# Optimization experiments

Hardware: AMD Instinct MI355X
Metric: run time of the kernel (lower is better)

## Reference

```python
import jax, jax.numpy as jnp
import numpy as np

N = 50000      # nodes per graph
E = 800000     # directed edges per graph
D_IN, C1, C2, C3, K = 96, 64, 32, 16, 16  # K = tensor_neurons (Linear(16,16) forces 16)


def setup_inputs() -> dict:
    key = jax.random.key(0)
    ks = jax.random.split(key, 18)
    def w(k, shape, scale=0.1):
        return (jax.random.normal(k, shape, jnp.float32) * scale)
    return {
        "features_1": jax.random.normal(ks[0], (N, D_IN), jnp.float32),
        "features_2": jax.random.normal(ks[1], (N, D_IN), jnp.float32),
        "edges_1": jax.random.randint(ks[2], (2, E), 0, N),
        "edges_2": jax.random.randint(ks[3], (2, E), 0, N),
        # GCN layer params (PyG GCNConv: X @ W then normalized aggregation, then + b)
        "W1": w(ks[4], (D_IN, C1)), "b1": jnp.zeros((C1,), jnp.float32),
        "W2": w(ks[5], (C1, C2)),  "b2": jnp.zeros((C2,), jnp.float32),
        "W3": w(ks[6], (C2, C3)),  "b3": jnp.zeros((C3,), jnp.float32),
        # Attention pooling weight matrix [C3, C3]
        "Wa": w(ks[7], (C3, C3)),
        # Tensor network: bilinear tensor [C3, C3, K], block [K, 2*C3], bias [K]
        "Wt": w(ks[8], (C3, C3, K)),
        "Wb": w(ks[9], (K, 2 * C3)),
        "bt": w(ks[10], (K,)),
        # fully_connected_first Linear(16,16) and scoring Linear(16,1)
        "Wfc": w(ks[11], (K, 16)), "bfc": jnp.zeros((16,), jnp.float32),
        "Wsc": w(ks[12], (16, 1)), "bsc": jnp.zeros((1,), jnp.float32),
    }


def gcn_conv(x, src, dst, W, b):
    # PyG GCNConv with self-loops: D^-1/2 (A+I) D^-1/2 (X W) + b
    h = x @ W                                   # [N, C]
    ones = jnp.ones(src.shape[0], h.dtype)
    deg = jax.ops.segment_sum(ones, dst, num_segments=N) + 1.0   # in-degree + self loop
    dinv = jax.lax.rsqrt(deg)                   # [N]
    coef = dinv[src] * dinv[dst]                # [E]
    agg = jax.ops.segment_sum(h[src] * coef[:, None], dst, num_segments=N)
    return agg + h * (dinv * dinv)[:, None] + b  # self-loop term has norm dinv_i^2


def encode(x, edges, W1, b1, W2, b2, W3, b3):
    src, dst = edges[0], edges[1]
    x = jax.nn.relu(gcn_conv(x, src, dst, W1, b1))  # dropout is a no-op in eval mode
    x = jax.nn.relu(gcn_conv(x, src, dst, W2, b2))
    return gcn_conv(x, src, dst, W3, b3)


def attention_pool(x, Wa):
    # SimGNN AttentionModule: c = tanh(mean(x Wa)); s = sigmoid(x c); rep = x^T s
    c = jnp.tanh(jnp.mean(x @ Wa, axis=0))      # [C3]
    s = jax.nn.sigmoid(x @ c)                   # [N]
    return x.T @ s                              # [C3]


def reference(features_1, features_2, edges_1, edges_2,
              W1, b1, W2, b2, W3, b3, Wa, Wt, Wb, bt, Wfc, bfc, Wsc, bsc):
    h1 = encode(features_1, edges_1, W1, b1, W2, b2, W3, b3)
    h2 = encode(features_2, edges_2, W1, b1, W2, b2, W3, b3)
    e1 = attention_pool(h1, Wa)                 # [C3]
    e2 = attention_pool(h2, Wa)                 # [C3]
    # Tensor network scoring
    bilinear = jnp.einsum('i,ijk,j->k', e1, Wt, e2)        # [K]
    block = Wb @ jnp.concatenate([e1, e2])                 # [K]
    scores = jax.nn.relu(bilinear + block + bt)            # [K]
    scores = jnp.tanh(scores @ Wfc + bfc)                  # [16]
    score = jax.nn.sigmoid(scores @ Wsc + bsc)             # [1]
    return score
```

## Files before the change

kernel.cpp:

```cpp
#include <hip/hip_runtime.h>
#include <hip/hip_bf16.h>

#define TPB 256
#define SH 6
#define BW 64

typedef unsigned short u16;
typedef __attribute__((ext_vector_type(8))) __bf16 bf16x8;
typedef __attribute__((ext_vector_type(4))) float f32x4;

__device__ __forceinline__ u16 f_to_bf(float f) {
    unsigned u = __float_as_uint(f);
    return (u16)((u + 0x7fff + ((u >> 16) & 1)) >> 16);
}
__device__ __forceinline__ void facc(float4& a, float4 v) {
    a.x += v.x; a.y += v.y; a.z += v.z; a.w += v.w;
}

__device__ __forceinline__ bool swz_block(int nblk, int& g, int& bx) {
    int blk = blockIdx.x;
    int j = blk & 7;
    g = j >> 2;
    bx = (blk >> 3) * 4 + (j & 3);
    return bx < nblk;
}

__device__ __forceinline__ void acc8_add(float* __restrict__ a, uint4 d) {
    a[0] += __uint_as_float(d.x << 16);
    a[1] += __uint_as_float(d.x & 0xffff0000u);
    a[2] += __uint_as_float(d.y << 16);
    a[3] += __uint_as_float(d.y & 0xffff0000u);
    a[4] += __uint_as_float(d.z << 16);
    a[5] += __uint_as_float(d.z & 0xffff0000u);
    a[6] += __uint_as_float(d.w << 16);
    a[7] += __uint_as_float(d.w & 0xffff0000u);
}

template <int C>
__device__ __forceinline__ void gather_sum16(const u16* __restrict__ HW,
                                             const int* __restrict__ col,
                                             int e, int c8, int ps, int pe,
                                             float* __restrict__ acc) {
    int p = ps;
    for (; p + 8 <= pe; p += 8) {
        int j[4];
        uint4 d[4];
#pragma unroll
        for (int r = 0; r < 4; r++) j[r] = col[p + 2 * r + e];
#pragma unroll
        for (int r = 0; r < 4; r++) d[r] = *(const uint4*)&HW[(size_t)j[r] * C + c8 * 8];
#pragma unroll
        for (int r = 0; r < 4; r++) acc8_add(acc, d[r]);
    }
    for (; p + 2 <= pe; p += 2) {
        int j = col[p + e];
        acc8_add(acc, *(const uint4*)&HW[(size_t)j * C + c8 * 8]);
    }
    if (p < pe && e == 0) {
        int j = col[p];
        acc8_add(acc, *(const uint4*)&HW[(size_t)j * C + c8 * 8]);
    }
}

__device__ __forceinline__ void red8(float* __restrict__ a, int mask, int width) {
#pragma unroll
    for (int i = 0; i < 8; i++) a[i] += __shfl_xor(a[i], mask, width);
}


__global__ void bucket_scatter_kernel(const int* __restrict__ e0, const int* __restrict__ e1,
                                      int E, int* __restrict__ bcur,
                                      int* __restrict__ ebuf0, int* __restrict__ ebuf1,
                                      int nbuk, int cap) {
    int g = blockIdx.y;
    const int* src = g ? e1 : e0;
    const int* dst = src + E;
    int* ebuf = g ? ebuf1 : ebuf0;
    int* bu = bcur + g * 1024;
    __shared__ int hist[1024];
    for (int t = threadIdx.x; t < 1024; t += TPB) hist[t] = 0;
    __syncthreads();
    int base = blockIdx.x * 4096;
    int pk[16], bk[16], rk[16];
#pragma unroll
    for (int k = 0; k < 16; k++) {
        int e = base + k * TPB + (int)threadIdx.x;
        bk[k] = -1;
        if (e < E) {
            int s = src[e], d = dst[e];
            int b = d >> SH;
            bk[k] = b;
            pk[k] = (s << SH) | (d & (BW - 1));
            rk[k] = atomicAdd(&hist[b], 1);
        }
    }
    __syncthreads();
    for (int t = threadIdx.x; t < nbuk; t += TPB) {
        int h = hist[t];
        hist[t] = h ? atomicAdd(&bu[t], h) : 0;
    }
    __syncthreads();
#pragma unroll
    for (int k = 0; k < 16; k++)
        if (bk[k] >= 0) {
            int pos = hist[bk[k]] + rk[k];
            if (pos < cap) ebuf[(size_t)bk[k] * cap + pos] = pk[k];
        }
}

__global__ void bucket_csr_kernel(const int* __restrict__ ebuf0, const int* __restrict__ ebuf1,
                                  const int* __restrict__ bcur, int n, int cap,
                                  int* __restrict__ soff0, int* __restrict__ soff1,
                                  int* __restrict__ eoff0, int* __restrict__ eoff1,
                                  float* __restrict__ dinv0, float* __restrict__ dinv1,
                                  int* __restrict__ col0, int* __restrict__ col1) {
    int g = blockIdx.y;
    int b = blockIdx.x;
    const int* ebuf = g ? ebuf1 : ebuf0;
    int* soff = g ? soff1 : soff0;
    int* eoff = g ? eoff1 : eoff0;
    float* dinv = g ? dinv1 : dinv0;
    int* col = g ? col1 : col0;
    __shared__ int h[BW], nb[BW], nrank[BW];
    int tid = threadIdx.x;
    if (tid < BW) h[tid] = 0;
    __syncthreads();
    int s = b * cap;
    int cnt = min(bcur[g * 1024 + b], cap);
    int e = s + cnt;
    for (int i = s + tid; i < e; i += TPB)
        atomicAdd(&h[ebuf[i] & (BW - 1)], 1);
    __syncthreads();
    if (tid < BW) {
        int v = h[tid];
        int x = v;
        for (int d = 1; d < BW; d <<= 1) {
            int u = __shfl_up(x, d, 64);
            if (tid >= d) x += u;
        }
        int base = s + x - v;
        nb[tid] = base;
        nrank[tid] = 0;
        int node = b * BW + tid;
        if (node < n) {
            soff[node] = base;
            eoff[node] = base + v;
            dinv[node] = rsqrtf((float)v + 1.0f);
        }
    }
    __syncthreads();
    for (int i = s + tid; i < e; i += TPB) {
        int p = ebuf[i];
        int lo = p & (BW - 1);
        int r = atomicAdd(&nrank[lo], 1);
        col[nb[lo] + r] = p >> SH;
    }
}


template <int CIN, int COUT>
__global__ void matmul_kernel(const float* __restrict__ X0, const float* __restrict__ X1,
                              const float* __restrict__ W,
                              const float* __restrict__ dinv0, const float* __restrict__ dinv1,
                              u16* __restrict__ Y0, u16* __restrict__ Y1, int n) {
    constexpr int CINP = CIN + 8;
    constexpr int NT = COUT / 16;
    constexpr int KT = CIN / 32;
    __shared__ u16 Xs[64 * CINP];
    __shared__ u16 Wt[COUT * CINP];

    int g = blockIdx.y;
    const float* X = g ? X1 : X0;
    const float* dinv = g ? dinv1 : dinv0;
    u16* Y = g ? Y1 : Y0;
    int nb0 = blockIdx.x * 64;

    for (int i = threadIdx.x; i < 64 * (CIN / 4); i += TPB) {
        int nn = i / (CIN / 4), kc = i % (CIN / 4);
        float4 v = make_float4(0.f, 0.f, 0.f, 0.f);
        if (nb0 + nn < n) v = *(const float4*)&X[(size_t)(nb0 + nn) * CIN + 4 * kc];
        ushort4 b;
        b.x = f_to_bf(v.x); b.y = f_to_bf(v.y); b.z = f_to_bf(v.z); b.w = f_to_bf(v.w);
        *(ushort4*)&Xs[nn * CINP + 4 * kc] = b;
    }
    for (int i = threadIdx.x; i < CIN * (COUT / 4); i += TPB) {
        int k = i / (COUT / 4), nc4 = i % (COUT / 4);
        float4 v = *(const float4*)&W[(size_t)k * COUT + 4 * nc4];
        Wt[(4 * nc4 + 0) * CINP + k] = f_to_bf(v.x);
        Wt[(4 * nc4 + 1) * CINP + k] = f_to_bf(v.y);
        Wt[(4 * nc4 + 2) * CINP + k] = f_to_bf(v.z);
        Wt[(4 * nc4 + 3) * CINP + k] = f_to_bf(v.w);
    }
    __syncthreads();

    int lane = threadIdx.x & 63;
    int w = threadIdx.x >> 6;
    int m = lane & 15;
    int quad = lane >> 4;

    f32x4 acc[NT];
#pragma unroll
    for (int t = 0; t < NT; t++) acc[t] = (f32x4){0.f, 0.f, 0.f, 0.f};
#pragma unroll
    for (int kt = 0; kt < KT; kt++) {
        int k0 = kt * 32 + quad * 8;
        bf16x8 a = *(const bf16x8*)&Xs[(w * 16 + m) * CINP + k0];
#pragma unroll
        for (int t = 0; t < NT; t++) {
            bf16x8 b = *(const bf16x8*)&Wt[(t * 16 + m) * CINP + k0];
            acc[t] = __builtin_amdgcn_mfma_f32_16x16x32_bf16(a, b, acc[t], 0, 0, 0);
        }
    }
#pragma unroll
    for (int r = 0; r < 4; r++) {
        int node = nb0 + w * 16 + quad * 4 + r;
        if (node < n) {
            float d = dinv[node];
#pragma unroll
            for (int t = 0; t < NT; t++)
                Y[(size_t)node * COUT + t * 16 + m] = f_to_bf(acc[t][r] * d);
        }
    }
}


template <int C, int SPLIT, int COUT2>
__global__ __launch_bounds__(TPB, 2)
void agg_mm_kernel(const u16* __restrict__ HW0, const u16* __restrict__ HW1,
                   const int* __restrict__ soff0, const int* __restrict__ soff1,
                   const int* __restrict__ eoff0, const int* __restrict__ eoff1,
                   const int* __restrict__ col0, const int* __restrict__ col1,
                   const float* __restrict__ dinv0, const float* __restrict__ dinv1,
                   const float* __restrict__ bias, const float* __restrict__ W2,
                   u16* __restrict__ Y0, u16* __restrict__ Y1, int n, int nblk) {
    constexpr int CHUNKS = C / 8;
    constexpr int GRP = 2 * CHUNKS;
    constexpr int TPN = GRP * SPLIT;
    constexpr int CP = C + 8;
    constexpr int NT2 = COUT2 / 16;
    constexpr int KT2 = C / 32;
    __shared__ __align__(16) u16 HsB[16 * CP];
    __shared__ __align__(16) u16 WtB[COUT2 * CP];

    int g, bx;
    if (!swz_block(nblk, g, bx)) return;
    const u16* HW = g ? HW1 : HW0;
    const int* soff = g ? soff1 : soff0;
    const int* eoff = g ? eoff1 : eoff0;
    const int* col = g ? col1 : col0;
    const float* dinv = g ? dinv1 : dinv0;
    u16* Y = g ? Y1 : Y0;

    for (int idx = threadIdx.x; idx < C * COUT2; idx += TPB) {
        int k = idx / COUT2, nc = idx % COUT2;
        WtB[nc * CP + k] = f_to_bf(W2[idx]);
    }

    int nl = threadIdx.x >> 4;
    int part = threadIdx.x & 15;
    int sp = part / GRP;
    int gl = part % GRP;
    int e = gl / CHUNKS;
    int c8 = gl % CHUNKS;
    int node = bx * 16 + nl;

    float acc[8];
#pragma unroll
    for (int i = 0; i < 8; i++) acc[i] = 0.f;
    float o8[8];
#pragma unroll
    for (int i = 0; i < 8; i++) o8[i] = 0.f;

    if (node < n) {
        int s = soff[node], en = eoff[node];
        int len = en - s;
        int chunk = (len + SPLIT - 1) / SPLIT;
        int ps = s + sp * chunk;
        int pe = min(ps + chunk, en);
        gather_sum16<C>(HW, col, e, c8, ps, pe, acc);
        red8(acc, CHUNKS, TPN);
#pragma unroll
        for (int m = GRP; m < TPN; m <<= 1) red8(acc, m, TPN);
        if (part < CHUNKS) {
            float di = dinv[node];
            uint4 sv = *(const uint4*)&HW[(size_t)node * C + part * 8];
            float4 b0 = *(const float4*)&bias[part * 8];
            float4 b1 = *(const float4*)&bias[part * 8 + 4];
            o8[0] = fmaxf(di * (acc[0] + __uint_as_float(sv.x << 16)) + b0.x, 0.f);
            o8[1] = fmaxf(di * (acc[1] + __uint_as_float(sv.x & 0xffff0000u)) + b0.y, 0.f);
            o8[2] = fmaxf(di * (acc[2] + __uint_as_float(sv.y << 16)) + b0.z, 0.f);
            o8[3] = fmaxf(di * (acc[3] + __uint_as_float(sv.y & 0xffff0000u)) + b0.w, 0.f);
            o8[4] = fmaxf(di * (acc[4] + __uint_as_float(sv.z << 16)) + b1.x, 0.f);
            o8[5] = fmaxf(di * (acc[5] + __uint_as_float(sv.z & 0xffff0000u)) + b1.y, 0.f);
            o8[6] = fmaxf(di * (acc[6] + __uint_as_float(sv.w << 16)) + b1.z, 0.f);
            o8[7] = fmaxf(di * (acc[7] + __uint_as_float(sv.w & 0xffff0000u)) + b1.w, 0.f);
        }
    }
    if (part < CHUNKS) {
        uint4 hv;
        hv.x = (unsigned)f_to_bf(o8[0]) | ((unsigned)f_to_bf(o8[1]) << 16);
        hv.y = (unsigned)f_to_bf(o8[2]) | ((unsigned)f_to_bf(o8[3]) << 16);
        hv.z = (unsigned)f_to_bf(o8[4]) | ((unsigned)f_to_bf(o8[5]) << 16);
        hv.w = (unsigned)f_to_bf(o8[6]) | ((unsigned)f_to_bf(o8[7]) << 16);
        *(uint4*)&HsB[nl * CP + part * 8] = hv;
    }
    __syncthreads();

    int lane = threadIdx.x & 63;
    int w = threadIdx.x >> 6;
    if (w < NT2) {
        int m = lane & 15;
        int quad = lane >> 4;
        f32x4 ac = (f32x4){0.f, 0.f, 0.f, 0.f};
#pragma unroll
        for (int kt = 0; kt < KT2; kt++) {
            int k0 = kt * 32 + quad * 8;
            bf16x8 a = *(const bf16x8*)&HsB[m * CP + k0];
            bf16x8 b = *(const bf16x8*)&WtB[(w * 16 + m) * CP + k0];
            ac = __builtin_amdgcn_mfma_f32_16x16x32_bf16(a, b, ac, 0, 0, 0);
        }
        int base16 = bx * 16;
#pragma unroll
        for (int r = 0; r < 4; r++) {
            int onode = base16 + quad * 4 + r;
            if (onode < n)
                Y[(size_t)onode * COUT2 + w * 16 + m] = f_to_bf(ac[r] * dinv[onode]);
        }
    }
}

__global__ __launch_bounds__(TPB, 2)
void agg16_kernel(const u16* __restrict__ HW0, const u16* __restrict__ HW1,
                  const int* __restrict__ soff0, const int* __restrict__ soff1,
                  const int* __restrict__ eoff0, const int* __restrict__ eoff1,
                  const int* __restrict__ col0, const int* __restrict__ col1,
                  const float* __restrict__ dinv0, const float* __restrict__ dinv1,
                  const float* __restrict__ bias,
                  u16* __restrict__ out0, u16* __restrict__ out1,
                  float* __restrict__ pcol, int n, int nblk) {
    int g, bx;
    if (!swz_block(nblk, g, bx)) return;
    const u16* HW = g ? HW1 : HW0;
    const int* soff = g ? soff1 : soff0;
    const int* eoff = g ? eoff1 : eoff0;
    const int* col = g ? col1 : col0;
    const float* dinv = g ? dinv1 : dinv0;
    u16* outp = g ? out1 : out0;

    int nl = threadIdx.x >> 4;
    int part = threadIdx.x & 15;
    int sp = part >> 2;
    int gl = part & 3;
    int e = gl >> 1;
    int c8 = gl & 1;
    int node = bx * 16 + nl;

    float acc[8];
#pragma unroll
    for (int i = 0; i < 8; i++) acc[i] = 0.f;
    float o8[8];
#pragma unroll
    for (int i = 0; i < 8; i++) o8[i] = 0.f;

    if (node < n) {
        int s = soff[node], en = eoff[node];
        int len = en - s;
        int chunk = (len + 3) >> 2;
        int ps = s + sp * chunk;
        int pe = min(ps + chunk, en);
        gather_sum16<16>(HW, col, e, c8, ps, pe, acc);
        red8(acc, 2, 16);
        red8(acc, 4, 16);
        red8(acc, 8, 16);
        if (part < 2) {
            float di = dinv[node];
            uint4 sv = *(const uint4*)&HW[(size_t)node * 16 + part * 8];
            float4 b0 = *(const float4*)&bias[part * 8];
            float4 b1 = *(const float4*)&bias[part * 8 + 4];
            o8[0] = di * (acc[0] + __uint_as_float(sv.x << 16)) + b0.x;
            o8[1] = di * (acc[1] + __uint_as_float(sv.x & 0xffff0000u)) + b0.y;
            o8[2] = di * (acc[2] + __uint_as_float(sv.y << 16)) + b0.z;
            o8[3] = di * (acc[3] + __uint_as_float(sv.y & 0xffff0000u)) + b0.w;
            o8[4] = di * (acc[4] + __uint_as_float(sv.z << 16)) + b1.x;
            o8[5] = di * (acc[5] + __uint_as_float(sv.z & 0xffff0000u)) + b1.y;
            o8[6] = di * (acc[6] + __uint_as_float(sv.w << 16)) + b1.z;
            o8[7] = di * (acc[7] + __uint_as_float(sv.w & 0xffff0000u)) + b1.w;
            uint4 hv;
            hv.x = (unsigned)f_to_bf(o8[0]) | ((unsigned)f_to_bf(o8[1]) << 16);
            hv.y = (unsigned)f_to_bf(o8[2]) | ((unsigned)f_to_bf(o8[3]) << 16);
            hv.z = (unsigned)f_to_bf(o8[4]) | ((unsigned)f_to_bf(o8[5]) << 16);
            hv.w = (unsigned)f_to_bf(o8[6]) | ((unsigned)f_to_bf(o8[7]) << 16);
            *(uint4*)&outp[(size_t)node * 16 + part * 8] = hv;
        }
    }
    __shared__ float4 sa[TPB], sb[TPB];
    bool hold = (node < n) && (part < 2);
    sa[threadIdx.x] = hold ? make_float4(o8[0], o8[1], o8[2], o8[3])
                           : make_float4(0.f, 0.f, 0.f, 0.f);
    sb[threadIdx.x] = hold ? make_float4(o8[4], o8[5], o8[6], o8[7])
                           : make_float4(0.f, 0.f, 0.f, 0.f);
    __syncthreads();
    if (threadIdx.x < 64) {
        float4 a = sa[threadIdx.x], b = sb[threadIdx.x];
        facc(a, sa[threadIdx.x + 64]);  facc(b, sb[threadIdx.x + 64]);
        facc(a, sa[threadIdx.x + 128]); facc(b, sb[threadIdx.x + 128]);
        facc(a, sa[threadIdx.x + 192]); facc(b, sb[threadIdx.x + 192]);
        sa[threadIdx.x] = a; sb[threadIdx.x] = b;
    }
    __syncthreads();
    if (threadIdx.x < 16) {
        float4 a = sa[threadIdx.x], b = sb[threadIdx.x];
        facc(a, sa[threadIdx.x + 16]); facc(b, sb[threadIdx.x + 16]);
        facc(a, sa[threadIdx.x + 32]); facc(b, sb[threadIdx.x + 32]);
        facc(a, sa[threadIdx.x + 48]); facc(b, sb[threadIdx.x + 48]);
        sa[threadIdx.x] = a; sb[threadIdx.x] = b;
    }
    __syncthreads();
    if (threadIdx.x < 2) {
        float* dst = &pcol[((size_t)g * nblk + bx) * 16 + threadIdx.x * 8];
        *(float4*)&dst[0] = sa[threadIdx.x];
        *(float4*)&dst[4] = sb[threadIdx.x];
    }
}


__global__ void cvec_kernel(const float* __restrict__ pcol, int nb16, float n_inv,
                            const float* __restrict__ Wa, float* __restrict__ cvec) {
    int g = blockIdx.x;
    const float4* p4 = (const float4*)(pcol + (size_t)g * nb16 * 16);
    __shared__ float4 sd[TPB];
    __shared__ float cs[16];
    int c4 = threadIdx.x & 3;
    int row = threadIdx.x >> 2;
    float4 acc = make_float4(0.f, 0.f, 0.f, 0.f);
    for (int r = row; r < nb16; r += 64) facc(acc, p4[(size_t)r * 4 + c4]);
    sd[threadIdx.x] = acc;
    __syncthreads();
    if (threadIdx.x < 64) {
        float4 a = sd[threadIdx.x];
        facc(a, sd[threadIdx.x + 64]);
        facc(a, sd[threadIdx.x + 128]);
        facc(a, sd[threadIdx.x + 192]);
        sd[threadIdx.x] = a;
    }
    __syncthreads();
    if (threadIdx.x < 16) {
        float4 a = sd[threadIdx.x];
        facc(a, sd[threadIdx.x + 16]);
        facc(a, sd[threadIdx.x + 32]);
        facc(a, sd[threadIdx.x + 48]);
        sd[threadIdx.x] = a;
    }
// ... 106 lines not shown
        tvec[t] = tanhf(acc);
    }
    __syncthreads();
    if (t == 0) {
        float acc = bsc[0];
#pragma unroll
        for (int j = 0; j < 16; j++) acc += tvec[j] * Wsc[j];
        out[0] = 1.f / (1.f + __expf(-acc));
    }
}


extern "C" void kernel_launch(void* const* d_in, const int* in_sizes, int n_in,
                              void* d_out, int out_size, void* d_ws, size_t ws_size,
                              hipStream_t stream) {
    const float* X1 = (const float*)d_in[0];
    const float* X2 = (const float*)d_in[1];
    const int* edges1 = (const int*)d_in[2];
    const int* edges2 = (const int*)d_in[3];
    const float* W1 = (const float*)d_in[4];
    const float* b1 = (const float*)d_in[5];
    const float* W2 = (const float*)d_in[6];
    const float* b2 = (const float*)d_in[7];
    const float* W3 = (const float*)d_in[8];
    const float* b3 = (const float*)d_in[9];
    const float* Wa = (const float*)d_in[10];
    const float* Wt = (const float*)d_in[11];
    const float* Wb = (const float*)d_in[12];
    const float* bt = (const float*)d_in[13];
    const float* Wfc = (const float*)d_in[14];
    const float* bfc = (const float*)d_in[15];
    const float* Wsc = (const float*)d_in[16];
    const float* bsc = (const float*)d_in[17];
    float* out = (float*)d_out;

    const int N = in_sizes[0] / 96;
    const int E = in_sizes[2] / 2;
    const int NBUK = (N + BW - 1) / BW;
    int cap = ((2 * (E / NBUK)) + 255) & ~255;
    if (cap < 256) cap = 256;

    char* ws = (char*)d_ws;
    size_t o = 0;
    auto alloc = [&](size_t bytes) {
        void* p = ws + o;
        o += (bytes + 255) & ~(size_t)255;
        return p;
    };
    int* bcur = (int*)alloc((size_t)2 * 1024 * 4);
    int* soff0 = (int*)alloc((size_t)N * 4);
    int* soff1 = (int*)alloc((size_t)N * 4);
    int* eoff0 = (int*)alloc((size_t)N * 4);
    int* eoff1 = (int*)alloc((size_t)N * 4);
    int* col0 = (int*)alloc((size_t)NBUK * cap * 4);
    int* col1 = (int*)alloc((size_t)NBUK * cap * 4);
    int* ebuf0 = (int*)alloc((size_t)NBUK * cap * 4);
    int* ebuf1 = (int*)alloc((size_t)NBUK * cap * 4);
    float* dinv0 = (float*)alloc((size_t)N * 4);
    float* dinv1 = (float*)alloc((size_t)N * 4);
    u16* hwbA0 = (u16*)alloc((size_t)N * 64 * 2);
    u16* hwbA1 = (u16*)alloc((size_t)N * 64 * 2);
    u16* hwbB0 = (u16*)alloc((size_t)N * 32 * 2);
    u16* hwbB1 = (u16*)alloc((size_t)N * 32 * 2);
    u16* hwbC0 = (u16*)alloc((size_t)N * 16 * 2);
    u16* hwbC1 = (u16*)alloc((size_t)N * 16 * 2);
    u16* H30 = (u16*)alloc((size_t)N * 16 * 2);
    u16* H31 = (u16*)alloc((size_t)N * 16 * 2);

    const int gB2 = (E + 4095) / 4096;
    const int g16 = ((size_t)N * 16 + TPB - 1) / TPB;
    const int gSwz = 8 * ((g16 + 3) / 4);
    const int gMM = (N + 63) / 64;
    const int gPool = 256;

    float* pcol = (float*)alloc((size_t)2 * g16 * 16 * 4);
    float* cvecArr = (float*)alloc(32 * 4);
    float* ppool = (float*)alloc((size_t)2 * gPool * 16 * 4);

    hipMemsetAsync(bcur, 0, (size_t)2 * 1024 * 4, stream);

    bucket_scatter_kernel<<<dim3(gB2, 2), TPB, 0, stream>>>(edges1, edges2, E, bcur,
                                                            ebuf0, ebuf1, NBUK, cap);
    bucket_csr_kernel<<<dim3(NBUK, 2), TPB, 0, stream>>>(ebuf0, ebuf1, bcur, N, cap,
                                                         soff0, soff1, eoff0, eoff1,
                                                         dinv0, dinv1, col0, col1);

    matmul_kernel<96, 64><<<dim3(gMM, 2), TPB, 0, stream>>>(X1, X2, W1, dinv0, dinv1,
                                                            hwbA0, hwbA1, N);
    agg_mm_kernel<64, 1, 32><<<gSwz, TPB, 0, stream>>>(
        hwbA0, hwbA1, soff0, soff1, eoff0, eoff1, col0, col1, dinv0, dinv1, b1, W2,
        hwbB0, hwbB1, N, g16);
    agg_mm_kernel<32, 2, 16><<<gSwz, TPB, 0, stream>>>(
        hwbB0, hwbB1, soff0, soff1, eoff0, eoff1, col0, col1, dinv0, dinv1, b2, W3,
        hwbC0, hwbC1, N, g16);
    agg16_kernel<<<gSwz, TPB, 0, stream>>>(
        hwbC0, hwbC1, soff0, soff1, eoff0, eoff1, col0, col1, dinv0, dinv1, b3,
        H30, H31, pcol, N, g16);

    cvec_kernel<<<2, TPB, 0, stream>>>(pcol, g16, 1.0f / (float)N, Wa, cvecArr);
    pool_kernel<<<dim3(gPool, 2), TPB, 0, stream>>>(H30, H31, N, cvecArr, ppool);
    final_kernel<<<1, 256, 0, stream>>>(ppool, gPool, Wt, Wb, bt, Wfc, bfc, Wsc, bsc, out);
}
```

Measured before the change: 256.7 us.

## Store intermediate GCN feature tables in FP8 and regroup gather threads

The per-layer transformed feature tables (X·W scaled by dinv) are now stored as FP8 instead of bf16, halving bytes per gathered neighbor row. Gather threads now load 16 channels per 16-byte load and process 4 edges in parallel per group, with the shuffle reductions adjusted to match. This is meant to cut memory traffic in the bandwidth-bound edge aggregations. The cost is extra conversion instructions and lower precision, which could hurt output accuracy.

Measured after the change: 272.4 us. +6.1%, slower.

```diff
diff --git a/kernel.cpp b/kernel.cpp
--- a/kernel.cpp
+++ b/kernel.cpp
@@ -6,6 +6,7 @@
 #define BW 64
 
 typedef unsigned short u16;
+typedef unsigned char u8;
 typedef __attribute__((ext_vector_type(8))) __bf16 bf16x8;
 typedef __attribute__((ext_vector_type(4))) float f32x4;
 
@@ -13,8 +14,35 @@
     unsigned u = __float_as_uint(f);
     return (u16)((u + 0x7fff + ((u >> 16) & 1)) >> 16);
 }
+__device__ __forceinline__ unsigned pkbf(float a, float b) {
+    return (unsigned)f_to_bf(a) | ((unsigned)f_to_bf(b) << 16);
+}
 __device__ __forceinline__ void facc(float4& a, float4 v) {
     a.x += v.x; a.y += v.y; a.z += v.z; a.w += v.w;
+}
+
+__device__ __forceinline__ u8 f_to_fp8(float f) {
+    return (u8)(__builtin_amdgcn_cvt_pk_fp8_f32(f, f, 0, false) & 0xff);
+}
+__device__ __forceinline__ void dec16(uint4 d, float* __restrict__ f) {
+    auto w = __builtin_amdgcn_cvt_pk_f32_fp8(d.x, false); f[0] = w[0]; f[1] = w[1];
+    w = __builtin_amdgcn_cvt_pk_f32_fp8(d.x, true);  f[2] = w[0];  f[3] = w[1];
+    w = __builtin_amdgcn_cvt_pk_f32_fp8(d.y, false); f[4] = w[0];  f[5] = w[1];
+    w = __builtin_amdgcn_cvt_pk_f32_fp8(d.y, true);  f[6] = w[0];  f[7] = w[1];
+    w = __builtin_amdgcn_cvt_pk_f32_fp8(d.z, false); f[8] = w[0];  f[9] = w[1];
+    w = __builtin_amdgcn_cvt_pk_f32_fp8(d.z, true);  f[10] = w[0]; f[11] = w[1];
+    w = __builtin_amdgcn_cvt_pk_f32_fp8(d.w, false); f[12] = w[0]; f[13] = w[1];
+    w = __builtin_amdgcn_cvt_pk_f32_fp8(d.w, true);  f[14] = w[0]; f[15] = w[1];
+}
+__device__ __forceinline__ void acc16_add(float* __restrict__ a, uint4 d) {
+    float t[16];
+    dec16(d, t);
+#pragma unroll
+    for (int i = 0; i < 16; i++) a[i] += t[i];
+}
+__device__ __forceinline__ void red16(float* __restrict__ a, int mask) {
+#pragma unroll
+    for (int i = 0; i < 16; i++) a[i] += __shfl_xor(a[i], mask, 16);
 }
 
 __device__ __forceinline__ bool swz_block(int nblk, int& g, int& bx) {
@@ -25,46 +53,30 @@
     return bx < nblk;
 }
 
-__device__ __forceinline__ void acc8_add(float* __restrict__ a, uint4 d) {
-    a[0] += __uint_as_float(d.x << 16);
-    a[1] += __uint_as_float(d.x & 0xffff0000u);
-    a[2] += __uint_as_float(d.y << 16);
-    a[3] += __uint_as_float(d.y & 0xffff0000u);
-    a[4] += __uint_as_float(d.z << 16);
-    a[5] += __uint_as_float(d.z & 0xffff0000u);
-    a[6] += __uint_as_float(d.w << 16);
-    a[7] += __uint_as_float(d.w & 0xffff0000u);
-}
-
-template <int C>
-__device__ __forceinline__ void gather_sum16(const u16* __restrict__ HW,
-                                             const int* __restrict__ col,
-                                             int e, int c8, int ps, int pe,
-                                             float* __restrict__ acc) {
+template <int CB, int EPG>
+__device__ __forceinline__ void gather_fp8(const u8* __restrict__ HW,
+                                           const int* __restrict__ col,
+                                           int e, int c16, int ps, int pe,
+                                           float* __restrict__ acc) {
     int p = ps;
-    for (; p + 8 <= pe; p += 8) {
+    for (; p + 4 * EPG <= pe; p += 4 * EPG) {
         int j[4];
         uint4 d[4];
 #pragma unroll
-        for (int r = 0; r < 4; r++) j[r] = col[p + 2 * r + e];
-#pragma unroll
-        for (int r = 0; r < 4; r++) d[r] = *(const uint4*)&HW[(size_t)j[r] * C + c8 * 8];
-#pragma unroll
-        for (int r = 0; r < 4; r++) acc8_add(acc, d[r]);
-    }
-    for (; p + 2 <= pe; p += 2) {
+        for (int r = 0; r < 4; r++) j[r] = col[p + EPG * r + e];
+#pragma unroll
+        for (int r = 0; r < 4; r++) d[r] = *(const uint4*)&HW[(size_t)j[r] * CB + c16 * 16];
+#pragma unroll
+        for (int r = 0; r < 4; r++) acc16_add(acc, d[r]);
+    }
+    for (; p + EPG <= pe; p += EPG) {
         int j = col[p + e];
-        acc8_add(acc, *(const uint4*)&HW[(size_t)j * C + c8 * 8]);
-    }
-    if (p < pe && e == 0) {
-        int j = col[p];
-        acc8_add(acc, *(const uint4*)&HW[(size_t)j * C + c8 * 8]);
-    }
-}
-
-__device__ __forceinline__ void red8(float* __restrict__ a, int mask, int width) {
-#pragma unroll
-    for (int i = 0; i < 8; i++) a[i] += __shfl_xor(a[i], mask, width);
+        acc16_add(acc, *(const uint4*)&HW[(size_t)j * CB + c16 * 16]);
+    }
+    if (p + e < pe) {
+        int j = col[p + e];
+        acc16_add(acc, *(const uint4*)&HW[(size_t)j * CB + c16 * 16]);
+    }
 }
 
 
@@ -162,7 +174,7 @@
 __global__ void matmul_kernel(const float* __restrict__ X0, const float* __restrict__ X1,
                               const float* __restrict__ W,
                               const float* __restrict__ dinv0, const float* __restrict__ dinv1,
-                              u16* __restrict__ Y0, u16* __restrict__ Y1, int n) {
+                              u8* __restrict__ Y0, u8* __restrict__ Y1, int n) {
     constexpr int CINP = CIN + 8;
     constexpr int NT = COUT / 16;
     constexpr int KT = CIN / 32;
@@ -172,7 +184,7 @@
     int g = blockIdx.y;
     const float* X = g ? X1 : X0;
     const float* dinv = g ? dinv1 : dinv0;
-    u16* Y = g ? Y1 : Y0;
+    u8* Y = g ? Y1 : Y0;
     int nb0 = blockIdx.x * 64;
 
     for (int i = threadIdx.x; i < 64 * (CIN / 4); i += TPB) {
@@ -218,24 +230,25 @@
             float d = dinv[node];
 #pragma unroll
             for (int t = 0; t < NT; t++)
-                Y[(size_t)node * COUT + t * 16 + m] = f_to_bf(acc[t][r] * d);
-        }
-    }
-}
-
-
-template <int C, int SPLIT, int COUT2>
+                Y[(size_t)node * COUT + t * 16 + m] = f_to_fp8(acc[t][r] * d);
+        }
+    }
+}
+
+
+template <int C, int COUT2>
 __global__ __launch_bounds__(TPB, 2)
-void agg_mm_kernel(const u16* __restrict__ HW0, const u16* __restrict__ HW1,
+void agg_mm_kernel(const u8* __restrict__ HW0, const u8* __restrict__ HW1,
                    const int* __restrict__ soff0, const int* __restrict__ soff1,
                    const int* __restrict__ eoff0, const int* __restrict__ eoff1,
                    const int* __restrict__ col0, const int* __restrict__ col1,
                    const float* __restrict__ dinv0, const float* __restrict__ dinv1,
                    const float* __restrict__ bias, const float* __restrict__ W2,
-                   u16* __restrict__ Y0, u16* __restrict__ Y1, int n, int nblk) {
-    constexpr int CHUNKS = C / 8;
-    constexpr int GRP = 2 * CHUNKS;
-    constexpr int TPN = GRP * SPLIT;
+                   u8* __restrict__ Y0, u8* __restrict__ Y1, int n, int nblk) {
+    constexpr int CHUNKS = C / 16;
+    constexpr int EPG = 4;
+    constexpr int GRP = EPG * CHUNKS;
+    constexpr int SPLIT = 16 / GRP;
     constexpr int CP = C + 8;
     constexpr int NT2 = COUT2 / 16;
     constexpr int KT2 = C / 32;
@@ -244,12 +257,12 @@
 
     int g, bx;
     if (!swz_block(nblk, g, bx)) return;
-    const u16* HW = g ? HW1 : HW0;
+    const u8* HW = g ? HW1 : HW0;
     const int* soff = g ? soff1 : soff0;
     const int* eoff = g ? eoff1 : eoff0;
     const int* col = g ? col1 : col0;
     const float* dinv = g ? dinv1 : dinv0;
-    u16* Y = g ? Y1 : Y0;
+    u8* Y = g ? Y1 : Y0;
 
     for (int idx = threadIdx.x; idx < C * COUT2; idx += TPB) {
         int k = idx / COUT2, nc = idx % COUT2;
@@ -261,15 +274,12 @@
     int sp = part / GRP;
     int gl = part % GRP;
     int e = gl / CHUNKS;
-    int c8 = gl % CHUNKS;
+    int c16 = gl % CHUNKS;
     int node = bx * 16 + nl;
 
-    float acc[8];
-#pragma unroll
-    for (int i = 0; i < 8; i++) acc[i] = 0.f;
-    float o8[8];
-#pragma unroll
-    for (int i = 0; i < 8; i++) o8[i] = 0.f;
+    float acc[16], o16[16];
+#pragma unroll
+    for (int i = 0; i < 16; i++) { acc[i] = 0.f; o16[i] = 0.f; }
 
     if (node < n) {
         int s = soff[node], en = eoff[node];
@@ -277,32 +287,26 @@
         int chunk = (len + SPLIT - 1) / SPLIT;
         int ps = s + sp * chunk;
         int pe = min(ps + chunk, en);
-        gather_sum16<C>(HW, col, e, c8, ps, pe, acc);
-        red8(acc, CHUNKS, TPN);
-#pragma unroll
-        for (int m = GRP; m < TPN; m <<= 1) red8(acc, m, TPN);
+        gather_fp8<C, EPG>(HW, col, e, c16, ps, pe, acc);
+#pragma unroll
+        for (int m = CHUNKS; m < 16; m <<= 1) red16(acc, m);
         if (part < CHUNKS) {
             float di = dinv[node];
-            uint4 sv = *(const uint4*)&HW[(size_t)node * C + part * 8];
-            float4 b0 = *(const float4*)&bias[part * 8];
-            float4 b1 = *(const float4*)&bias[part * 8 + 4];
-            o8[0] = fmaxf(di * (acc[0] + __uint_as_float(sv.x << 16)) + b0.x, 0.f);
-            o8[1] = fmaxf(di * (acc[1] + __uint_as_float(sv.x & 0xffff0000u)) + b0.y, 0.f);
-            o8[2] = fmaxf(di * (acc[2] + __uint_as_float(sv.y << 16)) + b0.z, 0.f);
-            o8[3] = fmaxf(di * (acc[3] + __uint_as_float(sv.y & 0xffff0000u)) + b0.w, 0.f);
-            o8[4] = fmaxf(di * (acc[4] + __uint_as_float(sv.z << 16)) + b1.x, 0.f);
-            o8[5] = fmaxf(di * (acc[5] + __uint_as_float(sv.z & 0xffff0000u)) + b1.y, 0.f);
-            o8[6] = fmaxf(di * (acc[6] + __uint_as_float(sv.w << 16)) + b1.z, 0.f);
-            o8[7] = fmaxf(di * (acc[7] + __uint_as_float(sv.w & 0xffff0000u)) + b1.w, 0.f);
+            float sv[16];
+            dec16(*(const uint4*)&HW[(size_t)node * C + part * 16], sv);
+#pragma unroll
+            for (int i = 0; i < 16; i++)
+                o16[i] = fmaxf(di * (acc[i] + sv[i]) + bias[part * 16 + i], 0.f);
         }
     }
     if (part < CHUNKS) {
-        uint4 hv;
-        hv.x = (unsigned)f_to_bf(o8[0]) | ((unsigned)f_to_bf(o8[1]) << 16);
-        hv.y = (unsigned)f_to_bf(o8[2]) | ((unsigned)f_to_bf(o8[3]) << 16);
-        hv.z = (unsigned)f_to_bf(o8[4]) | ((unsigned)f_to_bf(o8[5]) << 16);
-        hv.w = (unsigned)f_to_bf(o8[6]) | ((unsigned)f_to_bf(o8[7]) << 16);
-        *(uint4*)&HsB[nl * CP + part * 8] = hv;
+        uint4 h0, h1;
+        h0.x = pkbf(o16[0], o16[1]);   h0.y = pkbf(o16[2], o16[3]);
+        h0.z = pkbf(o16[4], o16[5]);   h0.w = pkbf(o16[6], o16[7]);
+        h1.x = pkbf(o16[8], o16[9]);   h1.y = pkbf(o16[10], o16[11]);
+        h1.z = pkbf(o16[12], o16[13]); h1.w = pkbf(o16[14], o16[15]);
+        *(uint4*)&HsB[nl * CP + part * 16] = h0;
+        *(uint4*)&HsB[nl * CP + part * 16 + 8] = h1;
     }
     __syncthreads();
 
@@ -324,13 +328,13 @@
         for (int r = 0; r < 4; r++) {
             int onode = base16 + quad * 4 + r;
             if (onode < n)
-                Y[(size_t)onode * COUT2 + w * 16 + m] = f_to_bf(ac[r] * dinv[onode]);
+                Y[(size_t)onode * COUT2 + w * 16 + m] = f_to_fp8(ac[r] * dinv[onode]);
         }
     }
 }
 
 __global__ __launch_bounds__(TPB, 2)
-void agg16_kernel(const u16* __restrict__ HW0, const u16* __restrict__ HW1,
+void agg16_kernel(const u8* __restrict__ HW0, const u8* __restrict__ HW1,
                   const int* __restrict__ soff0, const int* __restrict__ soff1,
                   const int* __restrict__ eoff0, const int* __restrict__ eoff1,
                   const int* __restrict__ col0, const int* __restrict__ col1,
@@ -338,9 +342,10 @@
                   const float* __restrict__ bias,
                   u16* __restrict__ out0, u16* __restrict__ out1,
                   float* __restrict__ pcol, int n, int nblk) {
+    constexpr int EPG = 4;
     int g, bx;
     if (!swz_block(nblk, g, bx)) return;
-    const u16* HW = g ? HW1 : HW0;
+    const u8* HW = g ? HW1 : HW0;
     const int* soff = g ? soff1 : soff0;
     const int* eoff = g ? eoff1 : eoff0;
     const int* col = g ? col1 : col0;
@@ -350,17 +355,12 @@
     int nl = threadIdx.x >> 4;
     int part = threadIdx.x & 15;
     int sp = part >> 2;
-    int gl = part & 3;
-    int e = gl >> 1;
-    int c8 = gl & 1;
+    int e = part & 3;
     int node = bx * 16 + nl;
 
-    float acc[8];
-#pragma unroll
-    for (int i = 0; i < 8; i++) acc[i] = 0.f;
-    float o8[8];
-#pragma unroll
-    for (int i = 0; i < 8; i++) o8[i] = 0.f;
+    float acc[16], o16[16];
+#pragma unroll
+    for (int i = 0; i < 16; i++) { acc[i] = 0.f; o16[i] = 0.f; }
 
     if (node < n) {
         int s = soff[node], en = eoff[node];
@@ -368,36 +368,38 @@
         int chunk = (len + 3) >> 2;
         int ps = s + sp * chunk;
         int pe = min(ps + chunk, en);
-        gather_sum16<16>(HW, col, e, c8, ps, pe, acc);
-        red8(acc, 2, 16);
-        red8(acc, 4, 16);
-        red8(acc, 8, 16);
-        if (part < 2) {
+        gather_fp8<16, EPG>(HW, col, e, 0, ps, pe, acc);
+        red16(acc, 1);
+        red16(acc, 2);
+        red16(acc, 4);
+        red16(acc, 8);
+        if (part == 0) {
             float di = dinv[node];
-            uint4 sv = *(const uint4*)&HW[(size_t)node * 16 + part * 8];
-            float4 b0 = *(const float4*)&bias[part * 8];
-            float4 b1 = *(const float4*)&bias[part * 8 + 4];
-            o8[0] = di * (acc[0] + __uint_as_float(sv.x << 16)) + b0.x;
-            o8[1] = di * (acc[1] + __uint_as_float(sv.x & 0xffff0000u)) + b0.y;
-            o8[2] = di * (acc[2] + __uint_as_float(sv.y << 16)) + b0.z;
-            o8[3] = di * (acc[3] + __uint_as_float(sv.y & 0xffff0000u)) + b0.w;
-            o8[4] = di * (acc[4] + __uint_as_float(sv.z << 16)) + b1.x;
-            o8[5] = di * (acc[5] + __uint_as_float(sv.z & 0xffff0000u)) + b1.y;
-            o8[6] = di * (acc[6] + __uint_as_float(sv.w << 16)) + b1.z;
-            o8[7] = di * (acc[7] + __uint_as_float(sv.w & 0xffff0000u)) + b1.w;
-            uint4 hv;
-            hv.x = (unsigned)f_to_bf(o8[0]) | ((unsigned)f_to_bf(o8[1]) << 16);
-            hv.y = (unsigned)f_to_bf(o8[2]) | ((unsigned)f_to_bf(o8[3]) << 16);
-            hv.z = (unsigned)f_to_bf(o8[4]) | ((unsigned)f_to_bf(o8[5]) << 16);
-            hv.w = (unsigned)f_to_bf(o8[6]) | ((unsigned)f_to_bf(o8[7]) << 16);
-            *(uint4*)&outp[(size_t)node * 16 + part * 8] = hv;
-        }
+            float sv[16];
+            dec16(*(const uint4*)&HW[(size_t)node * 16], sv);
+#pragma unroll
+            for (int i = 0; i < 16; i++)
+                o16[i] = di * (acc[i] + sv[i]) + bias[i];
+        }
+    }
+    float t8[8];
+#pragma unroll
+    for (int i = 0; i < 8; i++) t8[i] = __shfl(o16[8 + i], 0, 16);
+    float o8v[8];
+#pragma unroll
+    for (int i = 0; i < 8; i++) o8v[i] = (part == 0) ? o16[i] : t8[i];
+
+    if (node < n && part < 2) {
+        uint4 hv;
+        hv.x = pkbf(o8v[0], o8v[1]); hv.y = pkbf(o8v[2], o8v[3]);
+        hv.z = pkbf(o8v[4], o8v[5]); hv.w = pkbf(o8v[6], o8v[7]);
+        *(uint4*)&outp[(size_t)node * 16 + part * 8] = hv;
     }
     __shared__ float4 sa[TPB], sb[TPB];
     bool hold = (node < n) && (part < 2);
-    sa[threadIdx.x] = hold ? make_float4(o8[0], o8[1], o8[2], o8[3])
+    sa[threadIdx.x] = hold ? make_float4(o8v[0], o8v[1], o8v[2], o8v[3])
                            : make_float4(0.f, 0.f, 0.f, 0.f);
-    sb[threadIdx.x] = hold ? make_float4(o8[4], o8[5], o8[6], o8[7])
+    sb[threadIdx.x] = hold ? make_float4(o8v[4], o8v[5], o8v[6], o8v[7])
                            : make_float4(0.f, 0.f, 0.f, 0.f);
     __syncthreads();
     if (threadIdx.x < 64) {
@@ -616,12 +618,12 @@
     int* ebuf1 = (int*)alloc((size_t)NBUK * cap * 4);
     float* dinv0 = (float*)alloc((size_t)N * 4);
     float* dinv1 = (float*)alloc((size_t)N * 4);
-    u16* hwbA0 = (u16*)alloc((size_t)N * 64 * 2);
-    u16* hwbA1 = (u16*)alloc((size_t)N * 64 * 2);
-    u16* hwbB0 = (u16*)alloc((size_t)N * 32 * 2);
-    u16* hwbB1 = (u16*)alloc((size_t)N * 32 * 2);
-    u16* hwbC0 = (u16*)alloc((size_t)N * 16 * 2);
-    u16* hwbC1 = (u16*)alloc((size_t)N * 16 * 2);
+    u8* hwbA0 = (u8*)alloc((size_t)N * 64);
+    u8* hwbA1 = (u8*)alloc((size_t)N * 64);
+    u8* hwbB0 = (u8*)alloc((size_t)N * 32);
+    u8* hwbB1 = (u8*)alloc((size_t)N * 32);
+    u8* hwbC0 = (u8*)alloc((size_t)N * 16);
+    u8* hwbC1 = (u8*)alloc((size_t)N * 16);
     u16* H30 = (u16*)alloc((size_t)N * 16 * 2);
     u16* H31 = (u16*)alloc((size_t)N * 16 * 2);
 
@@ -645,10 +647,10 @@
 
     matmul_kernel<96, 64><<<dim3(gMM, 2), TPB, 0, stream>>>(X1, X2, W1, dinv0, dinv1,
                                                             hwbA0, hwbA1, N);
-    agg_mm_kernel<64, 1, 32><<<gSwz, TPB, 0, stream>>>(
+    agg_mm_kernel<64, 32><<<gSwz, TPB, 0, stream>>>(
         hwbA0, hwbA1, soff0, soff1, eoff0, eoff1, col0, col1, dinv0, dinv1, b1, W2,
         hwbB0, hwbB1, N, g16);
-    agg_mm_kernel<32, 2, 16><<<gSwz, TPB, 0, stream>>>(
+    agg_mm_kernel<32, 16><<<gSwz, TPB, 0, stream>>>(
         hwbB0, hwbB1, soff0, soff1, eoff0, eoff1, col0, col1, dinv0, dinv1, b2, W3,
         hwbC0, hwbC1, N, g16);
     agg16_kernel<<<gSwz, TPB, 0, stream>>>(
```

## Store CSR column indices as u16 and add dedicated 64-channel gather kernel

Applied to the files above, without the earlier changes.

CSR column indices are now stored as 16-bit values instead of 32-bit, halving index traffic in all three aggregation kernels and in CSR construction. The first aggregation layer gets a specialised kernel: each node uses 16 threads, 4 edge lanes by 4 channel chunks, with each thread loading two 16-byte chunks per neighbour and unrolling over 16 edges per iteration. The shuffle reduction is correspondingly shorter. The u16 indices only work while the node count stays below 65536, and the new mapping changes register pressure and the memory-level parallelism per thread.

Measured after the change: 262.0 us. 1.02x slower.

```diff
diff --git a/kernel.cpp b/kernel.cpp
--- a/kernel.cpp
+++ b/kernel.cpp
@@ -13,19 +13,14 @@
     unsigned u = __float_as_uint(f);
     return (u16)((u + 0x7fff + ((u >> 16) & 1)) >> 16);
 }
+__device__ __forceinline__ unsigned pkbf(float a, float b) {
+    return (unsigned)f_to_bf(a) | ((unsigned)f_to_bf(b) << 16);
+}
 __device__ __forceinline__ void facc(float4& a, float4 v) {
     a.x += v.x; a.y += v.y; a.z += v.z; a.w += v.w;
 }
 
-__device__ __forceinline__ bool swz_block(int nblk, int& g, int& bx) {
-    int blk = blockIdx.x;
-    int j = blk & 7;
-    g = j >> 2;
-    bx = (blk >> 3) * 4 + (j & 3);
-    return bx < nblk;
-}
-
-__device__ __forceinline__ void acc8_add(float* __restrict__ a, uint4 d) {
+__device__ __forceinline__ void bacc8(float* __restrict__ a, uint4 d) {
     a[0] += __uint_as_float(d.x << 16);
     a[1] += __uint_as_float(d.x & 0xffff0000u);
     a[2] += __uint_as_float(d.y << 16);
@@ -35,10 +30,38 @@
     a[6] += __uint_as_float(d.w << 16);
     a[7] += __uint_as_float(d.w & 0xffff0000u);
 }
+__device__ __forceinline__ void bdec8(uint4 d, float* __restrict__ f) {
+    f[0] = __uint_as_float(d.x << 16);
+    f[1] = __uint_as_float(d.x & 0xffff0000u);
+    f[2] = __uint_as_float(d.y << 16);
+    f[3] = __uint_as_float(d.y & 0xffff0000u);
+    f[4] = __uint_as_float(d.z << 16);
+    f[5] = __uint_as_float(d.z & 0xffff0000u);
+    f[6] = __uint_as_float(d.w << 16);
+    f[7] = __uint_as_float(d.w & 0xffff0000u);
+}
+__device__ __forceinline__ void red8(float* __restrict__ a, int mask, int width) {
+#pragma unroll
+    for (int i = 0; i < 8; i++) a[i] += __shfl_xor(a[i], mask, width);
+}
+__device__ __forceinline__ uint4 pack8(const float* __restrict__ o) {
+    uint4 h;
+    h.x = pkbf(o[0], o[1]); h.y = pkbf(o[2], o[3]);
+    h.z = pkbf(o[4], o[5]); h.w = pkbf(o[6], o[7]);
+    return h;
+}
+
+__device__ __forceinline__ bool swz_block(int nblk, int& g, int& bx) {
+    int blk = blockIdx.x;
+    int j = blk & 7;
+    g = j >> 2;
+    bx = (blk >> 3) * 4 + (j & 3);
+    return bx < nblk;
+}
 
 template <int C>
 __device__ __forceinline__ void gather_sum16(const u16* __restrict__ HW,
-                                             const int* __restrict__ col,
+                                             const u16* __restrict__ col,
                                              int e, int c8, int ps, int pe,
                                              float* __restrict__ acc) {
     int p = ps;
@@ -50,21 +73,16 @@
 #pragma unroll
         for (int r = 0; r < 4; r++) d[r] = *(const uint4*)&HW[(size_t)j[r] * C + c8 * 8];
 #pragma unroll
-        for (int r = 0; r < 4; r++) acc8_add(acc, d[r]);
+        for (int r = 0; r < 4; r++) bacc8(acc, d[r]);
     }
     for (; p + 2 <= pe; p += 2) {
         int j = col[p + e];
-        acc8_add(acc, *(const uint4*)&HW[(size_t)j * C + c8 * 8]);
+        bacc8(acc, *(const uint4*)&HW[(size_t)j * C + c8 * 8]);
     }
     if (p < pe && e == 0) {
         int j = col[p];
-        acc8_add(acc, *(const uint4*)&HW[(size_t)j * C + c8 * 8]);
-    }
-}
-
-__device__ __forceinline__ void red8(float* __restrict__ a, int mask, int width) {
-#pragma unroll
-    for (int i = 0; i < 8; i++) a[i] += __shfl_xor(a[i], mask, width);
+        bacc8(acc, *(const uint4*)&HW[(size_t)j * C + c8 * 8]);
+    }
 }
 
 
@@ -113,14 +131,14 @@
                                   int* __restrict__ soff0, int* __restrict__ soff1,
                                   int* __restrict__ eoff0, int* __restrict__ eoff1,
                                   float* __restrict__ dinv0, float* __restrict__ dinv1,
-                                  int* __restrict__ col0, int* __restrict__ col1) {
+                                  u16* __restrict__ col0, u16* __restrict__ col1) {
     int g = blockIdx.y;
     int b = blockIdx.x;
     const int* ebuf = g ? ebuf1 : ebuf0;
     int* soff = g ? soff1 : soff0;
     int* eoff = g ? eoff1 : eoff0;
     float* dinv = g ? dinv1 : dinv0;
-    int* col = g ? col1 : col0;
+    u16* col = g ? col1 : col0;
     __shared__ int h[BW], nb[BW], nrank[BW];
     int tid = threadIdx.x;
     if (tid < BW) h[tid] = 0;
@@ -153,7 +171,7 @@
         int p = ebuf[i];
         int lo = p & (BW - 1);
         int r = atomicAdd(&nrank[lo], 1);
-        col[nb[lo] + r] = p >> SH;
+        col[nb[lo] + r] = (u16)(p >> SH);
     }
 }
 
@@ -224,12 +242,118 @@
 }
 
 
+template <int COUT2>
+__global__ __launch_bounds__(TPB, 2)
+void agg_mm64_kernel(const u16* __restrict__ HW0, const u16* __restrict__ HW1,
+                     const int* __restrict__ soff0, const int* __restrict__ soff1,
+                     const int* __restrict__ eoff0, const int* __restrict__ eoff1,
+                     const u16* __restrict__ col0, const u16* __restrict__ col1,
+                     const float* __restrict__ dinv0, const float* __restrict__ dinv1,
+                     const float* __restrict__ bias, const float* __restrict__ W2,
+                     u16* __restrict__ Y0, u16* __restrict__ Y1, int n, int nblk) {
+    constexpr int C = 64;
+    constexpr int CP = C + 8;
+    constexpr int NT2 = COUT2 / 16;
+    constexpr int KT2 = C / 32;
+    __shared__ __align__(16) u16 HsB[16 * CP];
+    __shared__ __align__(16) u16 WtB[COUT2 * CP];
+
+    int g, bx;
+    if (!swz_block(nblk, g, bx)) return;
+    const u16* HW = g ? HW1 : HW0;
+    const int* soff = g ? soff1 : soff0;
+    const int* eoff = g ? eoff1 : eoff0;
+    const u16* col = g ? col1 : col0;
+    const float* dinv = g ? dinv1 : dinv0;
+    u16* Y = g ? Y1 : Y0;
+
+    for (int idx = threadIdx.x; idx < C * COUT2; idx += TPB) {
+        int k = idx / COUT2, nc = idx % COUT2;
+        WtB[nc * CP + k] = f_to_bf(W2[idx]);
+    }
+
+    int nl = threadIdx.x >> 4;
+    int part = threadIdx.x & 15;
+    int e = part & 3;
+    int cb = part >> 2;
+    int node = bx * 16 + nl;
+
+    float a0[8], a1[8], o0[8], o1[8];
+#pragma unroll
+    for (int i = 0; i < 8; i++) { a0[i] = 0.f; a1[i] = 0.f; o0[i] = 0.f; o1[i] = 0.f; }
+
+    if (node < n) {
+        int s = soff[node], en = eoff[node];
+        int p = s;
+        for (; p + 16 <= en; p += 16) {
+            int j[4];
+            uint4 d0[4], d1[4];
+#pragma unroll
+            for (int r = 0; r < 4; r++) j[r] = col[p + 4 * r + e];
+#pragma unroll
+            for (int r = 0; r < 4; r++) {
+                const u16* row = &HW[(size_t)j[r] * C];
+                d0[r] = *(const uint4*)&row[cb * 8];
+                d1[r] = *(const uint4*)&row[cb * 8 + 32];
+            }
+#pragma unroll
+            for (int r = 0; r < 4; r++) { bacc8(a0, d0[r]); bacc8(a1, d1[r]); }
+        }
+        for (int q = p + e; q < en; q += 4) {
+            const u16* row = &HW[(size_t)col[q] * C];
+            bacc8(a0, *(const uint4*)&row[cb * 8]);
+            bacc8(a1, *(const uint4*)&row[cb * 8 + 32]);
+        }
+        red8(a0, 1, 16); red8(a1, 1, 16);
+        red8(a0, 2, 16); red8(a1, 2, 16);
+        if (e == 0) {
+            float di = dinv[node];
+            float sv0[8], sv1[8];
+            bdec8(*(const uint4*)&HW[(size_t)node * C + cb * 8], sv0);
+            bdec8(*(const uint4*)&HW[(size_t)node * C + cb * 8 + 32], sv1);
+#pragma unroll
+            for (int i = 0; i < 8; i++) {
+                o0[i] = fmaxf(di * (a0[i] + sv0[i]) + bias[cb * 8 + i], 0.f);
+                o1[i] = fmaxf(di * (a1[i] + sv1[i]) + bias[cb * 8 + 32 + i], 0.f);
+            }
+        }
+    }
+    if (e == 0) {
+        *(uint4*)&HsB[nl * CP + cb * 8] = pack8(o0);
+        *(uint4*)&HsB[nl * CP + cb * 8 + 32] = pack8(o1);
+    }
+    __syncthreads();
+
+    int lane = threadIdx.x & 63;
+    int w = threadIdx.x >> 6;
+    if (w < NT2) {
+        int m = lane & 15;
+        int quad = lane >> 4;
+        f32x4 ac = (f32x4){0.f, 0.f, 0.f, 0.f};
+#pragma unroll
+        for (int kt = 0; kt < KT2; kt++) {
+            int k0 = kt * 32 + quad * 8;
+            bf16x8 a = *(const bf16x8*)&HsB[m * CP + k0];
+            bf16x8 b = *(const bf16x8*)&WtB[(w * 16 + m) * CP + k0];
+            ac = __builtin_amdgcn_mfma_f32_16x16x32_bf16(a, b, ac, 0, 0, 0);
+        }
+        int base16 = bx * 16;
+#pragma unroll
+        for (int r = 0; r < 4; r++) {
+            int onode = base16 + quad * 4 + r;
+            if (onode < n)
+                Y[(size_t)onode * COUT2 + w * 16 + m] = f_to_bf(ac[r] * dinv[onode]);
+        }
+    }
+}
+
+
 template <int C, int SPLIT, int COUT2>
 __global__ __launch_bounds__(TPB, 2)
 void agg_mm_kernel(const u16* __restrict__ HW0, const u16* __restrict__ HW1,
                    const int* __restrict__ soff0, const int* __restrict__ soff1,
                    const int* __restrict__ eoff0, const int* __restrict__ eoff1,
-                   const int* __restrict__ col0, const int* __restrict__ col1,
+                   const u16* __restrict__ col0, const u16* __restrict__ col1,
                    const float* __restrict__ dinv0, const float* __restrict__ dinv1,
                    const float* __restrict__ bias, const float* __restrict__ W2,
                    u16* __restrict__ Y0, u16* __restrict__ Y1, int n, int nblk) {
@@ -247,7 +371,7 @@
     const u16* HW = g ? HW1 : HW0;
     const int* soff = g ? soff1 : soff0;
     const int* eoff = g ? eoff1 : eoff0;
-    const int* col = g ? col1 : col0;
+    const u16* col = g ? col1 : col0;
     const float* dinv = g ? dinv1 : dinv0;
     u16* Y = g ? Y1 : Y0;
 
@@ -264,12 +388,9 @@
     int c8 = gl % CHUNKS;
     int node = bx * 16 + nl;
 
-    float acc[8];
-#pragma unroll
-    for (int i = 0; i < 8; i++) acc[i] = 0.f;
-    float o8[8];
-#pragma unroll
-    for (int i = 0; i < 8; i++) o8[i] = 0.f;
+    float acc[8], o8[8];
+#pragma unroll
+    for (int i = 0; i < 8; i++) { acc[i] = 0.f; o8[i] = 0.f; }
 
     if (node < n) {
         int s = soff[node], en = eoff[node];
@@ -283,26 +404,22 @@
         for (int m = GRP; m < TPN; m <<= 1) red8(acc, m, TPN);
         if (part < CHUNKS) {
             float di = dinv[node];
-            uint4 sv = *(const uint4*)&HW[(size_t)node * C + part * 8];
+            float sv[8];
+            bdec8(*(const uint4*)&HW[(size_t)node * C + part * 8], sv);
             float4 b0 = *(const float4*)&bias[part * 8];
             float4 b1 = *(const float4*)&bias[part * 8 + 4];
-            o8[0] = fmaxf(di * (acc[0] + __uint_as_float(sv.x << 16)) + b0.x, 0.f);
-            o8[1] = fmaxf(di * (acc[1] + __uint_as_float(sv.x & 0xffff0000u)) + b0.y, 0.f);
-            o8[2] = fmaxf(di * (acc[2] + __uint_as_float(sv.y << 16)) + b0.z, 0.f);
-            o8[3] = fmaxf(di * (acc[3] + __uint_as_float(sv.y & 0xffff0000u)) + b0.w, 0.f);
-            o8[4] = fmaxf(di * (acc[4] + __uint_as_float(sv.z << 16)) + b1.x, 0.f);
-            o8[5] = fmaxf(di * (acc[5] + __uint_as_float(sv.z & 0xffff0000u)) + b1.y, 0.f);
-            o8[6] = fmaxf(di * (acc[6] + __uint_as_float(sv.w << 16)) + b1.z, 0.f);
-            o8[7] = fmaxf(di * (acc[7] + __uint_as_float(sv.w & 0xffff0000u)) + b1.w, 0.f);
+            o8[0] = fmaxf(di * (acc[0] + sv[0]) + b0.x, 0.f);
+            o8[1] = fmaxf(di * (acc[1] + sv[1]) + b0.y, 0.f);
+            o8[2] = fmaxf(di * (acc[2] + sv[2]) + b0.z, 0.f);
+            o8[3] = fmaxf(di * (acc[3] + sv[3]) + b0.w, 0.f);
+            o8[4] = fmaxf(di * (acc[4] + sv[4]) + b1.x, 0.f);
+            o8[5] = fmaxf(di * (acc[5] + sv[5]) + b1.y, 0.f);
+            o8[6] = fmaxf(di * (acc[6] + sv[6]) + b1.z, 0.f);
+            o8[7] = fmaxf(di * (acc[7] + sv[7]) + b1.w, 0.f);
         }
     }
     if (part < CHUNKS) {
-        uint4 hv;
-        hv.x = (unsigned)f_to_bf(o8[0]) | ((unsigned)f_to_bf(o8[1]) << 16);
-        hv.y = (unsigned)f_to_bf(o8[2]) | ((unsigned)f_to_bf(o8[3]) << 16);
-        hv.z = (unsigned)f_to_bf(o8[4]) | ((unsigned)f_to_bf(o8[5]) << 16);
-        hv.w = (unsigned)f_to_bf(o8[6]) | ((unsigned)f_to_bf(o8[7]) << 16);
-        *(uint4*)&HsB[nl * CP + part * 8] = hv;
+        *(uint4*)&HsB[nl * CP + part * 8] = pack8(o8);
     }
     __syncthreads();
 
@@ -333,7 +450,7 @@
 void agg16_kernel(const u16* __restrict__ HW0, const u16* __restrict__ HW1,
                   const int* __restrict__ soff0, const int* __restrict__ soff1,
                   const int* __restrict__ eoff0, const int* __restrict__ eoff1,
-                  const int* __restrict__ col0, const int* __restrict__ col1,
+                  const u16* __restrict__ col0, const u16* __restrict__ col1,
                   const float* __restrict__ dinv0, const float* __restrict__ dinv1,
                   const float* __restrict__ bias,
                   u16* __restrict__ out0, u16* __restrict__ out1,
@@ -343,7 +460,7 @@
     const u16* HW = g ? HW1 : HW0;
     const int* soff = g ? soff1 : soff0;
     const int* eoff = g ? eoff1 : eoff0;
-    const int* col = g ? col1 : col0;
+    const u16* col = g ? col1 : col0;
     const float* dinv = g ? dinv1 : dinv0;
     u16* outp = g ? out1 : out0;
 
@@ -355,12 +472,9 @@
     int c8 = gl & 1;
     int node = bx * 16 + nl;
 
-    float acc[8];
-#pragma unroll
-    for (int i = 0; i < 8; i++) acc[i] = 0.f;
-    float o8[8];
-#pragma unroll
-    for (int i = 0; i < 8; i++) o8[i] = 0.f;
+    float acc[8], o8v[8];
+#pragma unroll
+    for (int i = 0; i < 8; i++) { acc[i] = 0.f; o8v[i] = 0.f; }
 
     if (node < n) {
         int s = soff[node], en = eoff[node];
@@ -374,30 +488,26 @@
         red8(acc, 8, 16);
         if (part < 2) {
             float di = dinv[node];
-            uint4 sv = *(const uint4*)&HW[(size_t)node * 16 + part * 8];
+            float sv[8];
+            bdec8(*(const uint4*)&HW[(size_t)node * 16 + part * 8], sv);
             float4 b0 = *(const float4*)&bias[part * 8];
             float4 b1 = *(const float4*)&bias[part * 8 + 4];
-            o8[0] = di * (acc[0] + __uint_as_float(sv.x << 16)) + b0.x;
-            o8[1] = di * (acc[1] + __uint_as_float(sv.x & 0xffff0000u)) + b0.y;
-            o8[2] = di * (acc[2] + __uint_as_float(sv.y << 16)) + b0.z;
-            o8[3] = di * (acc[3] + __uint_as_float(sv.y & 0xffff0000u)) + b0.w;
-            o8[4] = di * (acc[4] + __uint_as_float(sv.z << 16)) + b1.x;
-            o8[5] = di * (acc[5] + __uint_as_float(sv.z & 0xffff0000u)) + b1.y;
-            o8[6] = di * (acc[6] + __uint_as_float(sv.w << 16)) + b1.z;
-            o8[7] = di * (acc[7] + __uint_as_float(sv.w & 0xffff0000u)) + b1.w;
-            uint4 hv;
-            hv.x = (unsigned)f_to_bf(o8[0]) | ((unsigned)f_to_bf(o8[1]) << 16);
-            hv.y = (unsigned)f_to_bf(o8[2]) | ((unsigned)f_to_bf(o8[3]) << 16);
-            hv.z = (unsigned)f_to_bf(o8[4]) | ((unsigned)f_to_bf(o8[5]) << 16);
-            hv.w = (unsigned)f_to_bf(o8[6]) | ((unsigned)f_to_bf(o8[7]) << 16);
-            *(uint4*)&outp[(size_t)node * 16 + part * 8] = hv;
+            o8v[0] = di * (acc[0] + sv[0]) + b0.x;
+            o8v[1] = di * (acc[1] + sv[1]) + b0.y;
+            o8v[2] = di * (acc[2] + sv[2]) + b0.z;
+            o8v[3] = di * (acc[3] + sv[3]) + b0.w;
+            o8v[4] = di * (acc[4] + sv[4]) + b1.x;
+            o8v[5] = di * (acc[5] + sv[5]) + b1.y;
+            o8v[6] = di * (acc[6] + sv[6]) + b1.z;
+            o8v[7] = di * (acc[7] + sv[7]) + b1.w;
+            *(uint4*)&outp[(size_t)node * 16 + part * 8] = pack8(o8v);
         }
     }
     __shared__ float4 sa[TPB], sb[TPB];
     bool hold = (node < n) && (part < 2);
-    sa[threadIdx.x] = hold ? make_float4(o8[0], o8[1], o8[2], o8[3])
+    sa[threadIdx.x] = hold ? make_float4(o8v[0], o8v[1], o8v[2], o8v[3])
                            : make_float4(0.f, 0.f, 0.f, 0.f);
-    sb[threadIdx.x] = hold ? make_float4(o8[4], o8[5], o8[6], o8[7])
+    sb[threadIdx.x] = hold ? make_float4(o8v[4], o8v[5], o8v[6], o8v[7])
                            : make_float4(0.f, 0.f, 0.f, 0.f);
     __syncthreads();
     if (threadIdx.x < 64) {
@@ -610,8 +720,8 @@
     int* soff1 = (int*)alloc((size_t)N * 4);
     int* eoff0 = (int*)alloc((size_t)N * 4);
     int* eoff1 = (int*)alloc((size_t)N * 4);
-    int* col0 = (int*)alloc((size_t)NBUK * cap * 4);
-    int* col1 = (int*)alloc((size_t)NBUK * cap * 4);
+    u16* col0 = (u16*)alloc((size_t)NBUK * cap * 2);
+    u16* col1 = (u16*)alloc((size_t)NBUK * cap * 2);
     int* ebuf0 = (int*)alloc((size_t)NBUK * cap * 4);
     int* ebuf1 = (int*)alloc((size_t)NBUK * cap * 4);
     float* dinv0 = (float*)alloc((size_t)N * 4);
@@ -645,7 +755,7 @@
 
     matmul_kernel<96, 64><<<dim3(gMM, 2), TPB, 0, stream>>>(X1, X2, W1, dinv0, dinv1,
                                                             hwbA0, hwbA1, N);
-    agg_mm_kernel<64, 1, 32><<<gSwz, TPB, 0, stream>>>(
+    agg_mm64_kernel<32><<<gSwz, TPB, 0, stream>>>(
         hwbA0, hwbA1, soff0, soff1, eoff0, eoff1, col0, col1, dinv0, dinv1, b1, W2,
         hwbB0, hwbB1, N, g16);
     agg_mm_kernel<32, 2, 16><<<gSwz, TPB, 0, stream>>>(
```
